# Kernel optimization log

Measured on AMD Instinct MI355X. Metric: run time of the kernel, lower is better.

Reference implementation:

```python
import jax, jax.numpy as jnp
import numpy as np

H = 6  # hidden size == input size

def _lstm_layer(x_tbf, h0, c0, Wih, Whh, bih, bhh):
    # x_tbf: [T, B, F]; Wih: [4H, F]; Whh: [4H, H]; biases: [4H]
    b = bih + bhh
    def step(carry, xt):
        h, c = carry
        gates = xt @ Wih.T + h @ Whh.T + b  # [B, 4H]
        i, f, g, o = jnp.split(gates, 4, axis=-1)  # PyTorch gate order i,f,g,o
        i = jax.nn.sigmoid(i)
        f = jax.nn.sigmoid(f)
        g = jnp.tanh(g)
        o = jax.nn.sigmoid(o)
        c = f * c + i * g
        h = o * jnp.tanh(c)
        return (h, c), h
    (_, _), hs = jax.lax.scan(step, (h0, c0), x_tbf)
    return hs  # [T, B, H]

def setup_inputs() -> dict:
    key = jax.random.key(0)
    ks = jax.random.split(key, 9)
    B, T = 4096, 1024
    s = 1.0 / np.sqrt(H)  # PyTorch LSTM init: U(-1/sqrt(H), 1/sqrt(H))
    u = lambda k, shape: jax.random.uniform(k, shape, jnp.float32, -s, s)
    return {
        "x": jax.random.normal(ks[0], (B, T, 6), jnp.float32),
        "w_ih_l0": u(ks[1], (4 * H, 6)),
        "w_hh_l0": u(ks[2], (4 * H, H)),
        "b_ih_l0": u(ks[3], (4 * H,)),
        "b_hh_l0": u(ks[4], (4 * H,)),
        "w_ih_l1": u(ks[5], (4 * H, H)),
        "w_hh_l1": u(ks[6], (4 * H, H)),
        "b_ih_l1": u(ks[7], (4 * H,)),
        "b_hh_l1": u(ks[8], (4 * H,)),
    }

def reference(x, w_ih_l0, w_hh_l0, b_ih_l0, b_hh_l0, w_ih_l1, w_hh_l1, b_ih_l1, b_hh_l1):
    B = x.shape[0]
    x_t = jnp.transpose(x, (1, 0, 2))  # [T, B, 6]
    z = jnp.zeros((B, H), x.dtype)
    h1 = _lstm_layer(x_t, z, z, w_ih_l0, w_hh_l0, b_ih_l0, b_hh_l0)
    h2 = _lstm_layer(h1, z, z, w_ih_l1, w_hh_l1, b_ih_l1, b_hh_l1)
    return jnp.transpose(h2, (1, 0, 2))  # [B, T, H] (x[0] of nn.LSTM output)
```

## Files before the change

kernel.cpp:

```cpp
#include <hip/hip_runtime.h>

#define T_STEPS 1024

__device__ __forceinline__ float vexp2(float x) { return __builtin_amdgcn_exp2f(x); }
__device__ __forceinline__ float vrcp(float x)  { return __builtin_amdgcn_rcpf(x); }
__device__ __forceinline__ float sigm(float x) {
    return vrcp(1.0f + vexp2(x * -1.44269504088896340736f));
}
__device__ __forceinline__ float tanh_f(float x) {
    return fmaf(2.0f, sigm(2.0f * x), -1.0f);
}

#define SWZ_BCAST(v, s) \
    __int_as_float(__builtin_amdgcn_ds_swizzle(__float_as_int(v), ((s) << 5)))
#define SWZ_XOR8(v) \
    __int_as_float(__builtin_amdgcn_ds_swizzle(__float_as_int(v), ((8 << 10) | 0x1F)))

__global__ __launch_bounds__(256) void lstm2_kernel(
    const float* __restrict__ x,
    const float* __restrict__ wih0, const float* __restrict__ whh0,
    const float* __restrict__ bih0, const float* __restrict__ bhh0,
    const float* __restrict__ wih1, const float* __restrict__ whh1,
    const float* __restrict__ bih1, const float* __restrict__ bhh1,
    float* __restrict__ out, int Btot)
{
    const int tid = threadIdx.x;
    const int l   = tid & 31;
    const int b   = blockIdx.x * 8 + (tid >> 5);
    if (b >= Btot) return;

    const bool isL1 = (l & 16) != 0;
    const bool isGO = (l & 8) != 0;
    int j = l & 7; if (j > 5) j = 5;

    const int rA = isGO ? (12 + j) : j;
    const int rB = isGO ? (18 + j) : (6 + j);

    const float* wa  = isL1 ? wih1 : whh0;
    const float* wb  = isL1 ? whh1 : wih0;
    const float* bip = isL1 ? bih1 : bih0;
    const float* bhp = isL1 ? bhh1 : bhh0;

    float waA[6], waB[6], wbA[6], wbB[6];
#pragma unroll
    for (int k = 0; k < 6; ++k) {
        waA[k] = wa[rA * 6 + k]; waB[k] = wa[rB * 6 + k];
        wbA[k] = wb[rA * 6 + k]; wbB[k] = wb[rB * 6 + k];
    }
    const float bA = bip[rA] + bhp[rA];
    const float bB = bip[rB] + bhp[rB];

    float h0b[6], h1b[6];
#pragma unroll
    for (int k = 0; k < 6; ++k) { h0b[k] = 0.0f; h1b[k] = 0.0f; }
    float c = 0.0f;

    const float* px = x + (size_t)b * (T_STEPS * 6);
    float* ps = out + (size_t)b * (T_STEPS * 6) + (l - 16);
    const bool lstore = (l >= 16) && (l < 22);

    auto loadx = [&](int t, float v[6]) {
        const float2* p2 = reinterpret_cast<const float2*>(px + (size_t)t * 6);
        float2 a = p2[0], b2 = p2[1], c2 = p2[2];
        v[0] = a.x; v[1] = a.y; v[2] = b2.x; v[3] = b2.y; v[4] = c2.x; v[5] = c2.y;
    };

#define ITER(K, CUR, PF)                                                        \
    {                                                                           \
        int tn_ = (K) + 3; if (tn_ > T_STEPS - 1) tn_ = T_STEPS - 1;            \
        loadx(tn_, PF);                                                         \
        float gA = bA, gB = bB, hA = 0.0f, hB = 0.0f;                           \
        _Pragma("unroll")                                                       \
        for (int q = 0; q < 6; ++q) {                                           \
            float bin = isL1 ? h1b[q] : CUR[q];                                 \
            gA = fmaf(wbA[q], bin, gA);  gB = fmaf(wbB[q], bin, gB);            \
            hA = fmaf(waA[q], h0b[q], hA); hB = fmaf(waB[q], h0b[q], hB);       \
        }                                                                       \
        float sA = gA + hA, sB = gB + hB;                                       \
        float preA = isGO ? 2.0f * sA : sA;                                     \
        float tAct = sigm(preA);                                                \
        float aA = isGO ? fmaf(2.0f, tAct, -1.0f) : tAct;   \
        float aB = sigm(sB);                                 \
        float eA = SWZ_XOR8(aA);         \
        float eB = SWZ_XOR8(aB);         \
        c = fmaf(aB, c, aA * eA);                        \
        float hv = eB * tanh_f(c);                       \
        if ((K) >= 1 && lstore) ps[(size_t)((K) - 1) * 6] = hv;                 \
        h0b[0] = SWZ_BCAST(hv, 0);  h0b[1] = SWZ_BCAST(hv, 1);                  \
        h0b[2] = SWZ_BCAST(hv, 2);  h0b[3] = SWZ_BCAST(hv, 3);                  \
        h0b[4] = SWZ_BCAST(hv, 4);  h0b[5] = SWZ_BCAST(hv, 5);                  \
        h1b[0] = SWZ_BCAST(hv, 16); h1b[1] = SWZ_BCAST(hv, 17);                 \
        h1b[2] = SWZ_BCAST(hv, 18); h1b[3] = SWZ_BCAST(hv, 19);                 \
        h1b[4] = SWZ_BCAST(hv, 20); h1b[5] = SWZ_BCAST(hv, 21);                 \
    }

    float xA[6], xB[6], xC[6], xD[6];
    loadx(0, xA); loadx(1, xB); loadx(2, xC);

    ITER(0, xA, xD);
    if (isL1) c = 0.0f;
#pragma unroll
    for (int k = 0; k < 6; ++k) h1b[k] = 0.0f;

    for (int k = 1; k <= T_STEPS; k += 4) {
        ITER(k,     xB, xA);
        ITER(k + 1, xC, xB);
        ITER(k + 2, xD, xC);
        ITER(k + 3, xA, xD);
    }
#undef ITER
}

extern "C" void kernel_launch(void* const* d_in, const int* in_sizes, int n_in,
                              void* d_out, int out_size, void* d_ws, size_t ws_size,
                              hipStream_t stream)
{
    const float* x    = (const float*)d_in[0];
    const float* wih0 = (const float*)d_in[1];
    const float* whh0 = (const float*)d_in[2];
    const float* bih0 = (const float*)d_in[3];
    const float* bhh0 = (const float*)d_in[4];
    const float* wih1 = (const float*)d_in[5];
    const float* whh1 = (const float*)d_in[6];
    const float* bih1 = (const float*)d_in[7];
    const float* bhh1 = (const float*)d_in[8];
    float* out = (float*)d_out;

    const int Btot   = in_sizes[0] / (T_STEPS * 6);
    const int blocks = (Btot + 7) / 8;
    hipLaunchKernelGGL(lstm2_kernel, dim3(blocks), dim3(256), 0, stream,
                       x, wih0, whh0, bih0, bhh0, wih1, whh1, bih1, bhh1, out, Btot);
}
```

Measured before the change: 450.3 us.

## Map one batch row per wavefront with one gate per lane and DPP exchange

Each batch row now uses a full 64-lane wavefront instead of 32 lanes. Every lane computes a single gate row instead of two, so it does one sigmoid per step. The log2e scaling is folded into the weights and bias. Gate values are exchanged within each quad with DPP, and hidden states are broadcast with readlane into scalar registers instead of ds_swizzle. This is meant to shorten the serial per-step dependency chain through cheaper cross-lane moves and fewer transcendentals per lane. In exchange it doubles the lanes per row and halves the rows per block, which lowers batch throughput per wave, and readlane goes through SGPRs with possible hazard stalls.

New measurement: 542.0 us. 20.3% more time.

```diff
diff --git a/kernel.cpp b/kernel.cpp
--- a/kernel.cpp
+++ b/kernel.cpp
@@ -4,17 +4,11 @@
 
 __device__ __forceinline__ float vexp2(float x) { return __builtin_amdgcn_exp2f(x); }
 __device__ __forceinline__ float vrcp(float x)  { return __builtin_amdgcn_rcpf(x); }
-__device__ __forceinline__ float sigm(float x) {
-    return vrcp(1.0f + vexp2(x * -1.44269504088896340736f));
-}
-__device__ __forceinline__ float tanh_f(float x) {
-    return fmaf(2.0f, sigm(2.0f * x), -1.0f);
-}
 
-#define SWZ_BCAST(v, s) \
-    __int_as_float(__builtin_amdgcn_ds_swizzle(__float_as_int(v), ((s) << 5)))
-#define SWZ_XOR8(v) \
-    __int_as_float(__builtin_amdgcn_ds_swizzle(__float_as_int(v), ((8 << 10) | 0x1F)))
+#define DPPQ(v, PAT) \
+    __int_as_float(__builtin_amdgcn_update_dpp(0, __float_as_int(v), (PAT), 0xF, 0xF, true))
+#define RDL(v, LANE) \
+    __int_as_float(__builtin_amdgcn_readlane(__float_as_int(v), (LANE)))
 
 __global__ __launch_bounds__(256) void lstm2_kernel(
     const float* __restrict__ x,
@@ -24,74 +18,77 @@
     const float* __restrict__ bih1, const float* __restrict__ bhh1,
     float* __restrict__ out, int Btot)
 {
-    const int tid = threadIdx.x;
-    const int l   = tid & 31;
-    const int b   = blockIdx.x * 8 + (tid >> 5);
+    const int tid  = threadIdx.x;
+    const int lane = tid & 63;
+    const int b    = blockIdx.x * 4 + (tid >> 6);
     if (b >= Btot) return;
 
-    const bool isL1 = (l & 16) != 0;
-    const bool isGO = (l & 8) != 0;
-    int j = l & 7; if (j > 5) j = 5;
+    const int  l    = lane & 31;
+    const bool isL1 = lane >= 32;
+    const int  qj   = l >> 2;
+    const int  j    = (qj > 5) ? 5 : qj;
+    const int  g    = l & 3;
+    const int  r    = 6 * g + j;
 
-    const int rA = isGO ? (12 + j) : j;
-    const int rB = isGO ? (18 + j) : (6 + j);
+    const float* wa = isL1 ? wih1 : whh0;
+    const float* wb = isL1 ? whh1 : wih0;
+    const float* bi = isL1 ? bih1 : bih0;
+    const float* bh = isL1 ? bhh1 : bhh0;
 
-    const float* wa  = isL1 ? wih1 : whh0;
-    const float* wb  = isL1 ? whh1 : wih0;
-    const float* bip = isL1 ? bih1 : bih0;
-    const float* bhp = isL1 ? bhh1 : bhh0;
+    const float kS   = -1.44269504088896340736f * ((g == 2) ? 2.0f : 1.0f);
+    const float aMul = (g == 2) ? 2.0f : 1.0f;
+    const float aAdd = (g == 2) ? -1.0f : 0.0f;
 
-    float waA[6], waB[6], wbA[6], wbB[6];
+    float waS[6], wbS[6];
 #pragma unroll
     for (int k = 0; k < 6; ++k) {
-        waA[k] = wa[rA * 6 + k]; waB[k] = wa[rB * 6 + k];
-        wbA[k] = wb[rA * 6 + k]; wbB[k] = wb[rB * 6 + k];
+        waS[k] = wa[r * 6 + k] * kS;
+        wbS[k] = wb[r * 6 + k] * kS;
     }
-    const float bA = bip[rA] + bhp[rA];
-    const float bB = bip[rB] + bhp[rB];
+    const float bS = (bi[r] + bh[r]) * kS;
 
-    float h0b[6], h1b[6];
+    float h0u[6], h1u[6];
 #pragma unroll
-    for (int k = 0; k < 6; ++k) { h0b[k] = 0.0f; h1b[k] = 0.0f; }
+    for (int k = 0; k < 6; ++k) { h0u[k] = 0.0f; h1u[k] = 0.0f; }
     float c = 0.0f;
 
-    const float* px = x + (size_t)b * (T_STEPS * 6);
-    float* ps = out + (size_t)b * (T_STEPS * 6) + (l - 16);
-    const bool lstore = (l >= 16) && (l < 22);
+    const float* px = x   + (size_t)b * (T_STEPS * 6);
+    float*       ps = out + (size_t)b * (T_STEPS * 6) + j;
+    const bool lst = isL1 && (g == 0) && (qj < 6);
 
     auto loadx = [&](int t, float v[6]) {
         const float2* p2 = reinterpret_cast<const float2*>(px + (size_t)t * 6);
         float2 a = p2[0], b2 = p2[1], c2 = p2[2];
-        v[0] = a.x; v[1] = a.y; v[2] = b2.x; v[3] = b2.y; v[4] = c2.x; v[5] = c2.y;
+        v[0]=a.x; v[1]=a.y; v[2]=b2.x; v[3]=b2.y; v[4]=c2.x; v[5]=c2.y;
     };
 
-#define ITER(K, CUR, PF)                                                        \
-    {                                                                           \
-        int tn_ = (K) + 3; if (tn_ > T_STEPS - 1) tn_ = T_STEPS - 1;            \
-        loadx(tn_, PF);                                                         \
-        float gA = bA, gB = bB, hA = 0.0f, hB = 0.0f;                           \
-        _Pragma("unroll")                                                       \
-        for (int q = 0; q < 6; ++q) {                                           \
-            float bin = isL1 ? h1b[q] : CUR[q];                                 \
-            gA = fmaf(wbA[q], bin, gA);  gB = fmaf(wbB[q], bin, gB);            \
-            hA = fmaf(waA[q], h0b[q], hA); hB = fmaf(waB[q], h0b[q], hB);       \
-        }                                                                       \
-        float sA = gA + hA, sB = gB + hB;                                       \
-        float preA = isGO ? 2.0f * sA : sA;                                     \
-        float tAct = sigm(preA);                                                \
-        float aA = isGO ? fmaf(2.0f, tAct, -1.0f) : tAct;   \
-        float aB = sigm(sB);                                 \
-        float eA = SWZ_XOR8(aA);         \
-        float eB = SWZ_XOR8(aB);         \
-        c = fmaf(aB, c, aA * eA);                        \
-        float hv = eB * tanh_f(c);                       \
-        if ((K) >= 1 && lstore) ps[(size_t)((K) - 1) * 6] = hv;                 \
-        h0b[0] = SWZ_BCAST(hv, 0);  h0b[1] = SWZ_BCAST(hv, 1);                  \
-        h0b[2] = SWZ_BCAST(hv, 2);  h0b[3] = SWZ_BCAST(hv, 3);                  \
-        h0b[4] = SWZ_BCAST(hv, 4);  h0b[5] = SWZ_BCAST(hv, 5);                  \
-        h1b[0] = SWZ_BCAST(hv, 16); h1b[1] = SWZ_BCAST(hv, 17);                 \
-        h1b[2] = SWZ_BCAST(hv, 18); h1b[3] = SWZ_BCAST(hv, 19);                 \
-        h1b[4] = SWZ_BCAST(hv, 20); h1b[5] = SWZ_BCAST(hv, 21);                 \
+#define ITER(K, CUR, PF)                                                      \
+    {                                                                         \
+        int tn_ = (K) + 3; if (tn_ > T_STEPS - 1) tn_ = T_STEPS - 1;          \
+        loadx(tn_, PF);                                                       \
+        float eX = 0.0f, eA = bS, eH = 0.0f;                                  \
+        _Pragma("unroll")                                                     \
+        for (int q = 0; q < 6; ++q) {                                         \
+            eA = fmaf(waS[q], h0u[q], eA);                                    \
+            eH = fmaf(wbS[q], h1u[q], eH);                                    \
+            eX = fmaf(wbS[q], CUR[q], eX);                                    \
+        }                                                                     \
+        float e  = eA + (isL1 ? eH : eX);                                     \
+        float sg = vrcp(1.0f + vexp2(e));                                     \
+        float a  = fmaf(aMul, sg, aAdd);           \
+        float aI = DPPQ(a, 0x00);                                             \
+        float aF = DPPQ(a, 0x55);                                             \
+        float aG = DPPQ(a, 0xAA);                                             \
+        float aO = DPPQ(a, 0xFF);                                             \
+        c = fmaf(aF, c, aI * aG);                                             \
+        float th = fmaf(2.0f, vrcp(1.0f + vexp2(c * -2.88539008177792681f)),  \
+                        -1.0f);                                               \
+        float hv = aO * th;                                                   \
+        if ((K) >= 1 && lst) ps[(size_t)((K) - 1) * 6] = hv;                  \
+        h0u[0]=RDL(hv,0);  h0u[1]=RDL(hv,4);  h0u[2]=RDL(hv,8);               \
+        h0u[3]=RDL(hv,12); h0u[4]=RDL(hv,16); h0u[5]=RDL(hv,20);              \
+        h1u[0]=RDL(hv,32); h1u[1]=RDL(hv,36); h1u[2]=RDL(hv,40);              \
+        h1u[3]=RDL(hv,44); h1u[4]=RDL(hv,48); h1u[5]=RDL(hv,52);              \
     }
 
     float xA[6], xB[6], xC[6], xD[6];
@@ -100,7 +97,7 @@
     ITER(0, xA, xD);
     if (isL1) c = 0.0f;
 #pragma unroll
-    for (int k = 0; k < 6; ++k) h1b[k] = 0.0f;
+    for (int k = 0; k < 6; ++k) h1u[k] = 0.0f;
 
     for (int k = 1; k <= T_STEPS; k += 4) {
         ITER(k,     xB, xA);
@@ -127,7 +124,7 @@
     float* out = (float*)d_out;
 
     const int Btot   = in_sizes[0] / (T_STEPS * 6);
-    const int blocks = (Btot + 7) / 8;
+    const int blocks = (Btot + 3) / 4;
     hipLaunchKernelGGL(lstm2_kernel, dim3(blocks), dim3(256), 0, stream,
                        x, wih0, whh0, bih0, bhh0, wih1, whh1, bih1, bhh1, out, Btot);
 }
```
